# Performance work log

Measured on AMD Instinct MI355X. Metric: run time of the kernel, lower is better.

Reference implementation:

```python
import jax, jax.numpy as jnp
import numpy as np

NU, NI = 100000, 50000      # global embedding table sizes
U, I = 50000, 20000         # nodes in this subgraph
E = 400000                  # edges per direction
HID, H = 512, 8
D = HID // H                # out_feats per head = 64
NEG_SLOPE = 0.2


def setup_inputs() -> dict:
    key = jax.random.key(0)
    ks = jax.random.split(key, 16)
    s = 1.0 / np.sqrt(HID)
    a = 1.0 / np.sqrt(D)
    return {
        'u_gid': jax.random.randint(ks[0], (U,), 0, NU),
        'i_gid': jax.random.randint(ks[1], (I,), 0, NI),
        'src_u': jax.random.randint(ks[2], (E,), 0, U),
        'dst_i': jax.random.randint(ks[3], (E,), 0, I),
        'user_emb': jax.random.normal(ks[4], (NU, HID), jnp.float32) * 0.02,
        'item_emb': jax.random.normal(ks[5], (NI, HID), jnp.float32) * 0.02,
        # 'interact' (user -> item) GATConv params
        'W_ui': jax.random.normal(ks[6], (HID, HID), jnp.float32) * s,
        'al_ui': jax.random.normal(ks[7], (H, D), jnp.float32) * a,
        'ar_ui': jax.random.normal(ks[8], (H, D), jnp.float32) * a,
        'b_ui': jnp.zeros((HID,), jnp.float32),
        # 'interact_rev' (item -> user) GATConv params
        'W_iu': jax.random.normal(ks[9], (HID, HID), jnp.float32) * s,
        'al_iu': jax.random.normal(ks[10], (H, D), jnp.float32) * a,
        'ar_iu': jax.random.normal(ks[11], (H, D), jnp.float32) * a,
        'b_iu': jnp.zeros((HID,), jnp.float32),
    }


def gat_conv(h_src, h_dst, src, dst, W, attn_l, attn_r, bias, n_dst):
    """DGL GATConv (eval mode, allow_zero_in_degree): [n_dst, H, D]."""
    fs = (h_src @ W).reshape(-1, H, D)            # [Ns,H,D]
    fd = (h_dst @ W).reshape(-1, H, D)            # [Nd,H,D]
    el = jnp.sum(fs * attn_l, axis=-1)            # [Ns,H]
    er = jnp.sum(fd * attn_r, axis=-1)            # [Nd,H]
    e = jax.nn.leaky_relu(el[src] + er[dst], NEG_SLOPE)   # [E,H]
    # segment softmax over incoming edges of each destination
    emax = jax.ops.segment_max(e, dst, num_segments=n_dst)[dst]
    ex = jnp.exp(e - emax)                        # [E,H]
    denom = jax.ops.segment_sum(ex, dst, num_segments=n_dst)[dst]
    alpha = ex / denom                            # [E,H]
    msg = fs[src] * alpha[:, :, None]             # [E,H,D]
    out = jax.ops.segment_sum(msg, dst, num_segments=n_dst)  # zero for isolated dst
    return out + bias.reshape(1, H, D)


def reference(u_gid, i_gid, src_u, dst_i, user_emb, item_emb,
              W_ui, al_ui, ar_ui, b_ui, W_iu, al_iu, ar_iu, b_iu):
    h_u0 = user_emb[u_gid]                        # [U,HID]
    h_i0 = item_emb[i_gid]                        # [I,HID]
    # 'interact': user -> item
    h_item = gat_conv(h_u0, h_i0, src_u, dst_i, W_ui, al_ui, ar_ui, b_ui, I)
    # 'interact_rev': item -> user (reversed edges)
    h_user = gat_conv(h_i0, h_u0, dst_i, src_u, W_iu, al_iu, ar_iu, b_iu, U)
    h_user = h_user.reshape(U, HID)
    h_item = h_item.reshape(I, HID)
    item_mean = jnp.mean(h_item, axis=0, keepdims=True)        # [1,HID]
    item_expand = jnp.broadcast_to(item_mean, (U, HID))
    return jnp.concatenate([h_user, item_expand], axis=1)      # [U, 2*HID]
```

## Files before the change

### kernel.cpp

```cpp
#include <hip/hip_runtime.h>
#include <hip/hip_bf16.h>
#include <stdint.h>

#define U_NODES 50000
#define I_NODES 20000
#define N_NODES 70000
#define M_PAD   70016
#define E_EDGES 400000
#define HID     512

typedef __attribute__((ext_vector_type(8))) short short8;
typedef __attribute__((ext_vector_type(4))) float floatx4;

static __device__ __forceinline__ uint16_t f2b(float f) {
    uint32_t x = __float_as_uint(f);
    x += 0x7fffu + ((x >> 16) & 1u);
    return (uint16_t)(x >> 16);
}
static __device__ __forceinline__ float b2f(short u) {
    return __uint_as_float(((uint32_t)(uint16_t)u) << 16);
}

__global__ void gather_cast(const int* __restrict__ u_gid, const int* __restrict__ i_gid,
                            const float* __restrict__ user_emb, const float* __restrict__ item_emb,
                            uint16_t* __restrict__ Xb)
{
    int t = blockIdx.x * 256 + threadIdx.x;
    int n = t >> 7;
    int j = (t & 127) << 2;
    uint2 o;
    if (n < N_NODES) {
        const float* src = (n < U_NODES) ? (user_emb + (size_t)u_gid[n] * HID)
                                         : (item_emb + (size_t)i_gid[n - U_NODES] * HID);
        float4 v = *(const float4*)(src + j);
        o.x = (uint32_t)f2b(v.x) | ((uint32_t)f2b(v.y) << 16);
        o.y = (uint32_t)f2b(v.z) | ((uint32_t)f2b(v.w) << 16);
    } else { o.x = 0u; o.y = 0u; }
    *(uint2*)(Xb + (size_t)n * HID + j) = o;
}

__global__ void prep_w(const float* __restrict__ Wui, const float* __restrict__ Wiu,
                       uint16_t* __restrict__ Wt)
{
    int t = blockIdx.x * 256 + threadIdx.x;
    int n = t >> 9, k = t & 511;
    float v = (n < 512) ? Wui[k * 512 + n] : Wiu[k * 512 + (n - 512)];
    Wt[(size_t)n * 512 + k] = f2b(v);
}

__global__ __launch_bounds__(256) void gemm_bf16(const uint16_t* __restrict__ Xb,
                                                 const uint16_t* __restrict__ Wt,
                                                 const float* __restrict__ al_ui, const float* __restrict__ ar_ui,
                                                 const float* __restrict__ al_iu, const float* __restrict__ ar_iu,
                                                 uint16_t* __restrict__ F,
                                                 float* __restrict__ ELui, float* __restrict__ ERui,
                                                 float* __restrict__ ELiu, float* __restrict__ ERiu)
{
    __shared__ __align__(16) uint16_t As[2][128 * 32];
    __shared__ __align__(16) uint16_t Bs[2][128 * 32];
    const int tid = threadIdx.x;
    const int wave = tid >> 6, lane = tid & 63;

    int bid = blockIdx.x;
    int x = bid & 7, ii = bid >> 3;
    int L = x * 547 + ii;
    const int m0 = (L >> 3) * 128;
    const int n0 = (L & 7) * 128;
    const int wm = (wave & 1) * 64;
    const int wn = (wave >> 1) * 64;

    const int rl2 = lane >> 2;
    const int sg = ((lane & 3) ^ ((lane >> 3) & 3)) * 8;
    const int ca = wave * 2, cb = wave * 2 + 1;
    const uint16_t* gA0 = Xb + (size_t)(m0 + ca * 16 + rl2) * HID + sg;
    const uint16_t* gA1 = Xb + (size_t)(m0 + cb * 16 + rl2) * HID + sg;
    const uint16_t* gB0 = Wt + (size_t)(n0 + ca * 16 + rl2) * HID + sg;
    const uint16_t* gB1 = Wt + (size_t)(n0 + cb * 16 + rl2) * HID + sg;

    floatx4 zero = {0.f, 0.f, 0.f, 0.f};
    floatx4 acc[4][4];
    #pragma unroll
    for (int a = 0; a < 4; ++a)
        #pragma unroll
        for (int b = 0; b < 4; ++b) acc[a][b] = zero;

    const int r = lane & 15, quad = lane >> 4;
    const int slq8 = (quad ^ ((r >> 1) & 3)) * 8;

#define STAGE(KO, BUF) do {                                                                         \
    __builtin_amdgcn_global_load_lds((const __attribute__((address_space(1))) void*)(gA0 + (KO)),   \
                                     (__attribute__((address_space(3))) void*)(&As[BUF][ca * 512]), 16, 0, 0); \
    __builtin_amdgcn_global_load_lds((const __attribute__((address_space(1))) void*)(gA1 + (KO)),   \
                                     (__attribute__((address_space(3))) void*)(&As[BUF][cb * 512]), 16, 0, 0); \
    __builtin_amdgcn_global_load_lds((const __attribute__((address_space(1))) void*)(gB0 + (KO)),   \
                                     (__attribute__((address_space(3))) void*)(&Bs[BUF][ca * 512]), 16, 0, 0); \
    __builtin_amdgcn_global_load_lds((const __attribute__((address_space(1))) void*)(gB1 + (KO)),   \
                                     (__attribute__((address_space(3))) void*)(&Bs[BUF][cb * 512]), 16, 0, 0); \
} while (0)

#define COMPUTE(BUF) do {                                                                           \
    short8 af[4], bf[4];                                                                            \
    _Pragma("unroll")                                                                               \
    for (int tm = 0; tm < 4; ++tm)                                                                  \
        af[tm] = *(const short8*)&As[BUF][(wm + tm * 16 + r) * 32 + slq8];                          \
    _Pragma("unroll")                                                                               \
    for (int tn = 0; tn < 4; ++tn)                                                                  \
        bf[tn] = *(const short8*)&Bs[BUF][(wn + tn * 16 + r) * 32 + slq8];                          \
    _Pragma("unroll")                                                                               \
    for (int tm = 0; tm < 4; ++tm)                                                                  \
        _Pragma("unroll")                                                                           \
        for (int tn = 0; tn < 4; ++tn)                                                              \
            acc[tm][tn] = __builtin_amdgcn_mfma_f32_16x16x32_bf16(af[tm], bf[tn], acc[tm][tn], 0, 0, 0); \
} while (0)

    STAGE(0, 0);
    __syncthreads();
    #pragma unroll
    for (int t = 0; t < 15; ++t) {
        const int bc = t & 1;
        STAGE((t + 1) * 32, bc ^ 1);
        COMPUTE(bc);
        __syncthreads();
    }
    COMPUTE(1);

#undef STAGE
#undef COMPUTE

    const bool collo = (n0 < 512);
    const bool allU = (m0 + 128 <= U_NODES);
    const bool allI = (m0 >= U_NODES);
    const bool storeb = (allU && collo) || (allI && !collo) || (!allU && !allI);

    const int colh = n0 + wn;
    const int h = (colh & 511) >> 6;
    const float* arv = collo ? ar_ui : ar_iu;
    float* ERp = collo ? ERui : ERiu;
    float ar4[4];
    #pragma unroll
    for (int tn = 0; tn < 4; ++tn) ar4[tn] = arv[h * 64 + tn * 16 + r];

    if (storeb) {
        const float* alv = collo ? al_ui : al_iu;
        float* ELp = collo ? ELui : ELiu;
        float al4[4];
        #pragma unroll
        for (int tn = 0; tn < 4; ++tn) al4[tn] = alv[h * 64 + tn * 16 + r];
        #pragma unroll
        for (int tm = 0; tm < 4; ++tm) {
            #pragma unroll
            for (int rr = 0; rr < 4; ++rr) {
                int row = m0 + wm + tm * 16 + quad * 4 + rr;
                float sl = 0.f, sr = 0.f;
                #pragma unroll
                for (int tn = 0; tn < 4; ++tn) {
                    sl += acc[tm][tn][rr] * al4[tn];
                    sr += acc[tm][tn][rr] * ar4[tn];
                }
                if (row < N_NODES && ((row < U_NODES) == collo)) {
                    #pragma unroll
                    for (int tn = 0; tn < 4; ++tn) {
                        int col = n0 + wn + tn * 16 + r;
                        F[(size_t)row * 1024 + col] = f2b(acc[tm][tn][rr]);
                    }
                }
                #pragma unroll
                for (int d = 1; d < 16; d <<= 1) {
                    sl += __shfl_xor(sl, d);
                    sr += __shfl_xor(sr, d);
                }
                if (r == 0 && row < N_NODES) {
                    ELp[row * 8 + h] = sl;
                    ERp[row * 8 + h] = sr;
                }
            }
        }
    } else {
        #pragma unroll
        for (int tm = 0; tm < 4; ++tm) {
            #pragma unroll
            for (int rr = 0; rr < 4; ++rr) {
                int row = m0 + wm + tm * 16 + quad * 4 + rr;
                float sr = 0.f;
                #pragma unroll
                for (int tn = 0; tn < 4; ++tn) sr += acc[tm][tn][rr] * ar4[tn];
                #pragma unroll
                for (int d = 1; d < 16; d <<= 1) sr += __shfl_xor(sr, d);
                if (r == 0 && row < N_NODES) ERp[row * 8 + h] = sr;
            }
        }
    }
}

__global__ void hist_kernel(const int* __restrict__ src_u, const int* __restrict__ dst_i,
                            int* __restrict__ counts_i, int* __restrict__ counts_u)
{
    int e = blockIdx.x * 256 + threadIdx.x;
    if (e >= E_EDGES) return;
    atomicAdd(&counts_i[dst_i[e]], 1);
    atomicAdd(&counts_u[src_u[e]], 1);
}

__global__ __launch_bounds__(1024) void scan_kernel(const int* __restrict__ counts_i,
                                                    const int* __restrict__ counts_u,
                                                    int* __restrict__ offs_i, int* __restrict__ cur_i,
                                                    int* __restrict__ offs_u, int* __restrict__ cur_u)
{
    const int* counts; int n; int* offs; int* cur;
    if (blockIdx.x == 0) { counts = counts_i; n = I_NODES; offs = offs_i; cur = cur_i; }
    else                 { counts = counts_u; n = U_NODES; offs = offs_u; cur = cur_u; }
    __shared__ int wsum[16];
    int tid = threadIdx.x, lane = tid & 63, w = tid >> 6;
    int carry = 0;
    for (int base = 0; base < n; base += 1024) {
        int i = base + tid;
        int v = (i < n) ? counts[i] : 0;
        int x = v;
        #pragma unroll
        for (int d = 1; d < 64; d <<= 1) {
            int y = __shfl_up(x, d, 64);
            if (lane >= d) x += y;
        }
        if (lane == 63) wsum[w] = x;
        __syncthreads();
        if (w == 0) {
            int s = (lane < 16) ? wsum[lane] : 0;
            #pragma unroll
            for (int d = 1; d < 16; d <<= 1) {
                int y = __shfl_up(s, d, 16);
                if ((lane & 15) >= d) s += y;
            }
            if (lane < 16) wsum[lane] = s;
        }
        __syncthreads();
        int wexcl = (w == 0) ? 0 : wsum[w - 1];
        int excl = carry + wexcl + (x - v);
        if (i < n) { offs[i] = excl; cur[i] = excl; }
        int tot = wsum[15];
        __syncthreads();
        carry += tot;
    }
    if (tid == 0) offs[n] = carry;
}

__global__ void scatter_kernel(const int* __restrict__ src_u, const int* __restrict__ dst_i,
                               int* __restrict__ cur_i, int* __restrict__ cur_u,
                               int* __restrict__ sorted_ui, int* __restrict__ sorted_iu,
                               const float* __restrict__ ELui, const float* __restrict__ ERui,
                               const float* __restrict__ ELiu, const float* __restrict__ ERiu,
                               float* __restrict__ ex_ui, float* __restrict__ ex_iu)
{
    int e = blockIdx.x * 256 + threadIdx.x;
    if (e >= E_EDGES) return;
    int s = src_u[e], d = dst_i[e];
    int dn = U_NODES + d;
    int p = atomicAdd(&cur_i[d], 1);
    int q = atomicAdd(&cur_u[s], 1);
    sorted_ui[p] = s;
    sorted_iu[q] = dn;
    #pragma unroll
    for (int h = 0; h < 8; ++h) {
        float e1 = ELui[s * 8 + h] + ERui[dn * 8 + h];
        e1 = (e1 >= 0.f) ? e1 : 0.2f * e1;
        ex_ui[(size_t)p * 8 + h] = __expf(e1);
        float e2 = ELiu[dn * 8 + h] + ERiu[s * 8 + h];
        e2 = (e2 >= 0.f) ? e2 : 0.2f * e2;
        ex_iu[(size_t)q * 8 + h] = __expf(e2);
    }
}

#define IBLK ((I_NODES + 3) / 4)
#define UBLK ((U_NODES + 3) / 4)
__global__ __launch_bounds__(256) void agg3_kernel(
    const int* __restrict__ offs_i, const int* __restrict__ sorted_ui, const float* __restrict__ ex_ui,
    const int* __restrict__ offs_u, const int* __restrict__ sorted_iu, const float* __restrict__ ex_iu,
    const uint16_t* __restrict__ F, const float* __restrict__ b_iu,
    float* __restrict__ out, float* __restrict__ itemF)
{
    int bid = blockIdx.x;
    int w = threadIdx.x >> 6, lane = threadIdx.x & 63;
    bool item_mode = bid < IBLK;
    const int* offs; const int* srcs; const float* ex; int dst, colbase, n_dst;
    if (item_mode) { offs = offs_i; srcs = sorted_ui; ex = ex_ui; dst = bid * 4 + w;          colbase = 0;   n_dst = I_NODES; }
    else           { offs = offs_u; srcs = sorted_iu; ex = ex_iu; dst = (bid - IBLK) * 4 + w; colbase = 512; n_dst = U_NODES; }
    if (dst >= n_dst) return;
    int h = lane >> 3;
    int j0 = offs[dst], j1 = offs[dst + 1];

    float den = 0.f;
    float acc[8] = {0.f, 0.f, 0.f, 0.f, 0.f, 0.f, 0.f, 0.f};
    const int fb = colbase + lane * 8;
    int j = j0;
    for (; j + 8 <= j1; j += 8) {
        int s[8]; float wt[8]; short8 f[8];
        #pragma unroll
        for (int i = 0; i < 8; ++i) s[i] = srcs[j + i];
        #pragma unroll
        for (int i = 0; i < 8; ++i) wt[i] = ex[(size_t)(j + i) * 8 + h];
        #pragma unroll
        for (int i = 0; i < 8; ++i) f[i] = *(const short8*)&F[(size_t)s[i] * 1024 + fb];
        #pragma unroll
        for (int i = 0; i < 8; ++i) {
            den += wt[i];
            #pragma unroll
            for (int q = 0; q < 8; ++q) acc[q] += wt[i] * b2f(f[i][q]);
        }
    }
    for (; j + 4 <= j1; j += 4) {
        int s[4]; float wt[4]; short8 f[4];
        #pragma unroll
        for (int i = 0; i < 4; ++i) s[i] = srcs[j + i];
        #pragma unroll
        for (int i = 0; i < 4; ++i) wt[i] = ex[(size_t)(j + i) * 8 + h];
        #pragma unroll
        for (int i = 0; i < 4; ++i) f[i] = *(const short8*)&F[(size_t)s[i] * 1024 + fb];
        #pragma unroll
        for (int i = 0; i < 4; ++i) {
            den += wt[i];
            #pragma unroll
            for (int q = 0; q < 8; ++q) acc[q] += wt[i] * b2f(f[i][q]);
        }
    }
    for (; j < j1; ++j) {
        int s0 = srcs[j];
        float w0 = ex[(size_t)j * 8 + h];
        short8 f0 = *(const short8*)&F[(size_t)s0 * 1024 + fb];
        den += w0;
        #pragma unroll
        for (int q = 0; q < 8; ++q) acc[q] += w0 * b2f(f0[q]);
    }
    float inv = (j1 > j0) ? (1.f / den) : 0.f;
    #pragma unroll
    for (int q = 0; q < 8; ++q) acc[q] *= inv;

    int col = lane * 8;
    if (item_mode) {
        float* o = itemF + (size_t)dst * 512 + col;
        float4 v0 = {acc[0], acc[1], acc[2], acc[3]};
        float4 v1 = {acc[4], acc[5], acc[6], acc[7]};
        *(float4*)(o + 0) = v0;
        *(float4*)(o + 4) = v1;
    } else {
        float* o = out + (size_t)dst * 1024 + col;
        float4 v0 = {acc[0] + b_iu[col + 0], acc[1] + b_iu[col + 1],
                     acc[2] + b_iu[col + 2], acc[3] + b_iu[col + 3]};
        float4 v1 = {acc[4] + b_iu[col + 4], acc[5] + b_iu[col + 5],
                     acc[6] + b_iu[col + 6], acc[7] + b_iu[col + 7]};
        *(float4*)(o + 0) = v0;
        *(float4*)(o + 4) = v1;
    }
}

__global__ void item_reduce(const float* __restrict__ itemF, float* __restrict__ partial2)
{
    int b = blockIdx.x;
    int t = threadIdx.x;
    int cg = (t & 127) * 4;
    int rp = t >> 7;
    float4 s = {0.f, 0.f, 0.f, 0.f};
    int r0 = b * 500;
    for (int r = r0 + rp; r < r0 + 500; r += 2) {
        float4 v = *(const float4*)&itemF[(size_t)r * 512 + cg];
        s.x += v.x; s.y += v.y; s.z += v.z; s.w += v.w;
    }
    *(float4*)&partial2[(size_t)(b * 2 + rp) * 512 + cg] = s;
}

__global__ void meanvec_kernel(const float* __restrict__ partial2, const float* __restrict__ b_ui,
                               float* __restrict__ mean_vec)
{
    int c = threadIdx.x;
    float s = 0.f;
    for (int p = 0; p < 80; ++p) s += partial2[p * 512 + c];
    mean_vec[c] = s * (1.0f / (float)I_NODES) + b_ui[c];
}

__global__ void bcast_kernel(const float* __restrict__ mean_vec, float* __restrict__ out)
{
    int t = blockIdx.x * 256 + threadIdx.x;
    int u = t >> 7, q = t & 127;
    float4 v = ((const float4*)mean_vec)[q];
    *(float4*)(out + (size_t)u * 1024 + 512 + q * 4) = v;
}

extern "C" void kernel_launch(void* const* d_in, const int* in_sizes, int n_in,
                              void* d_out, int out_size, void* d_ws, size_t ws_size,
                              hipStream_t stream)
{
    const int*   u_gid    = (const int*)d_in[0];
    const int*   i_gid    = (const int*)d_in[1];
    const int*   src_u    = (const int*)d_in[2];
    const int*   dst_i    = (const int*)d_in[3];
    const float* user_emb = (const float*)d_in[4];
    const float* item_emb = (const float*)d_in[5];
    const float* W_ui     = (const float*)d_in[6];
    const float* al_ui    = (const float*)d_in[7];
    const float* ar_ui    = (const float*)d_in[8];
    const float* b_ui     = (const float*)d_in[9];
    const float* W_iu     = (const float*)d_in[10];
    const float* al_iu    = (const float*)d_in[11];
    const float* ar_iu    = (const float*)d_in[12];
    const float* b_iu     = (const float*)d_in[13];
    float* out = (float*)d_out;

    char* ws = (char*)d_ws;
    size_t off = 0;
    auto alloc = [&](size_t bytes) -> void* {
        void* p = ws + off;
        off = (off + bytes + 255) & ~(size_t)255;
        return p;
    };
    uint16_t* Xb   = (uint16_t*)alloc((size_t)M_PAD * 512 * 2);
    uint16_t* Wt   = (uint16_t*)alloc((size_t)1024 * 512 * 2);
    uint16_t* F    = (uint16_t*)alloc((size_t)M_PAD * 1024 * 2);
    float* ELui    = (float*)alloc((size_t)N_NODES * 8 * 4);
    float* ERui    = (float*)alloc((size_t)N_NODES * 8 * 4);
    float* ELiu    = (float*)alloc((size_t)N_NODES * 8 * 4);
    float* ERiu    = (float*)alloc((size_t)N_NODES * 8 * 4);
    int* offs_i    = (int*)alloc((size_t)(I_NODES + 1) * 4);
    int* cur_i     = (int*)alloc((size_t)I_NODES * 4);
    int* offs_u    = (int*)alloc((size_t)(U_NODES + 1) * 4);
    int* cur_u     = (int*)alloc((size_t)U_NODES * 4);
    int* sorted_ui = (int*)alloc((size_t)E_EDGES * 4);
    int* sorted_iu = (int*)alloc((size_t)E_EDGES * 4);
    float* ex_ui   = (float*)alloc((size_t)E_EDGES * 8 * 4);
    float* ex_iu   = (float*)alloc((size_t)E_EDGES * 8 * 4);
    float* itemF   = (float*)alloc((size_t)I_NODES * 512 * 4);
    float* partial2= (float*)alloc((size_t)80 * 512 * 4);
    char* zptr = ws + off;
    int*   counts_i = (int*)alloc((size_t)I_NODES * 4);
    int*   counts_u = (int*)alloc((size_t)U_NODES * 4);
    size_t zbytes = (size_t)((ws + off) - zptr);
    float* mean_vec = (float*)alloc(512 * 4);
    (void)ws_size; (void)in_sizes; (void)n_in; (void)out_size;

    hipMemsetAsync(zptr, 0, zbytes, stream);
    prep_w<<<2048, 256, 0, stream>>>(W_ui, W_iu, Wt);
    gather_cast<<<M_PAD * 128 / 256, 256, 0, stream>>>(u_gid, i_gid, user_emb, item_emb, Xb);
    gemm_bf16<<<(M_PAD / 128) * 8, 256, 0, stream>>>(Xb, Wt, al_ui, ar_ui, al_iu, ar_iu,
                                                     F, ELui, ERui, ELiu, ERiu);
    hist_kernel<<<(E_EDGES + 255) / 256, 256, 0, stream>>>(src_u, dst_i, counts_i, counts_u);
    scan_kernel<<<2, 1024, 0, stream>>>(counts_i, counts_u, offs_i, cur_i, offs_u, cur_u);
    scatter_kernel<<<(E_EDGES + 255) / 256, 256, 0, stream>>>(src_u, dst_i, cur_i, cur_u,
                                                              sorted_ui, sorted_iu,
                                                              ELui, ERui, ELiu, ERiu,
                                                              ex_ui, ex_iu);
    agg3_kernel<<<IBLK + UBLK, 256, 0, stream>>>(offs_i, sorted_ui, ex_ui,
                                                 offs_u, sorted_iu, ex_iu,
                                                 F, b_iu, out, itemF);
    item_reduce<<<40, 256, 0, stream>>>(itemF, partial2);
    meanvec_kernel<<<1, 512, 0, stream>>>(partial2, b_ui, mean_vec);
    bcast_kernel<<<U_NODES * 128 / 256, 256, 0, stream>>>(mean_vec, out);
}
```

Measured before the change: 880.1 us.

## Recompute edge attention in aggregation, parallelize scan, widen item reduction

Drops the per-edge exp buffers written by the scatter kernel; the aggregation kernel now recomputes leaky-relu/exp weights from per-node EL/ER tables using the destination's ER value. The two-block serial prefix scan is replaced with a three-pass multi-block scan, and the item mean reduction uses four times as many blocks. This removes a large per-edge write/read and a serialized scan, at the cost of extra gathers of source EL values and redundant exp per lane in aggregation.

Measured after the change: 775.9 us. 1.13x faster.

```diff
diff --git a/kernel.cpp b/kernel.cpp
--- a/kernel.cpp
+++ b/kernel.cpp
@@ -201,91 +201,128 @@
     atomicAdd(&counts_u[src_u[e]], 1);
 }
 
-__global__ __launch_bounds__(1024) void scan_kernel(const int* __restrict__ counts_i,
-                                                    const int* __restrict__ counts_u,
-                                                    int* __restrict__ offs_i, int* __restrict__ cur_i,
-                                                    int* __restrict__ offs_u, int* __restrict__ cur_u)
-{
-    const int* counts; int n; int* offs; int* cur;
-    if (blockIdx.x == 0) { counts = counts_i; n = I_NODES; offs = offs_i; cur = cur_i; }
-    else                 { counts = counts_u; n = U_NODES; offs = offs_u; cur = cur_u; }
-    __shared__ int wsum[16];
-    int tid = threadIdx.x, lane = tid & 63, w = tid >> 6;
-    int carry = 0;
-    for (int base = 0; base < n; base += 1024) {
-        int i = base + tid;
-        int v = (i < n) ? counts[i] : 0;
-        int x = v;
-        #pragma unroll
-        for (int d = 1; d < 64; d <<= 1) {
-            int y = __shfl_up(x, d, 64);
-            if (lane >= d) x += y;
-        }
-        if (lane == 63) wsum[w] = x;
-        __syncthreads();
-        if (w == 0) {
-            int s = (lane < 16) ? wsum[lane] : 0;
-            #pragma unroll
-            for (int d = 1; d < 16; d <<= 1) {
-                int y = __shfl_up(s, d, 16);
-                if ((lane & 15) >= d) s += y;
-            }
-            if (lane < 16) wsum[lane] = s;
-        }
-        __syncthreads();
-        int wexcl = (w == 0) ? 0 : wsum[w - 1];
-        int excl = carry + wexcl + (x - v);
+#define SCAN_CHUNK 1024
+#define IBLKS ((I_NODES + SCAN_CHUNK - 1) / SCAN_CHUNK)
+#define UBLKS ((U_NODES + SCAN_CHUNK - 1) / SCAN_CHUNK)
+
+__global__ __launch_bounds__(256) void scan_level1(const int* __restrict__ counts_i,
+                                                   const int* __restrict__ counts_u,
+                                                   int* __restrict__ bsum)
+{
+    int b = blockIdx.x, t = threadIdx.x;
+    const int* cnt; int n, base;
+    if (b < IBLKS) { cnt = counts_i; n = I_NODES; base = b * SCAN_CHUNK; }
+    else           { cnt = counts_u; n = U_NODES; base = (b - IBLKS) * SCAN_CHUNK; }
+    int idx = base + t * 4;
+    int s = 0;
+    #pragma unroll
+    for (int k = 0; k < 4; ++k) { int i = idx + k; if (i < n) s += cnt[i]; }
+    __shared__ int ws[4];
+    int lane = t & 63, w = t >> 6;
+    int xv = s;
+    #pragma unroll
+    for (int d = 1; d < 64; d <<= 1) xv += __shfl_xor(xv, d);
+    if (lane == 0) ws[w] = xv;
+    __syncthreads();
+    if (t == 0) bsum[b] = ws[0] + ws[1] + ws[2] + ws[3];
+}
+
+__global__ void scan_level2(const int* __restrict__ bsum, int* __restrict__ boff,
+                            int* __restrict__ offs_i, int* __restrict__ offs_u)
+{
+    int t = threadIdx.x;
+    int w = t >> 6, lane = t & 63;
+    if (w == 0) {
+        int v = (lane < IBLKS) ? bsum[lane] : 0;
+        int xv = v;
+        #pragma unroll
+        for (int d = 1; d < 64; d <<= 1) { int y = __shfl_up(xv, d, 64); if (lane >= d) xv += y; }
+        if (lane < IBLKS) boff[lane] = xv - v;
+        if (lane == IBLKS - 1) offs_i[I_NODES] = xv;
+    } else {
+        int v = (lane < UBLKS) ? bsum[IBLKS + lane] : 0;
+        int xv = v;
+        #pragma unroll
+        for (int d = 1; d < 64; d <<= 1) { int y = __shfl_up(xv, d, 64); if (lane >= d) xv += y; }
+        if (lane < UBLKS) boff[IBLKS + lane] = xv - v;
+        if (lane == UBLKS - 1) offs_u[U_NODES] = xv;
+    }
+}
+
+__global__ __launch_bounds__(256) void scan_level3(const int* __restrict__ counts_i,
+                                                   const int* __restrict__ counts_u,
+                                                   const int* __restrict__ boff,
+                                                   int* __restrict__ offs_i, int* __restrict__ cur_i,
+                                                   int* __restrict__ offs_u, int* __restrict__ cur_u)
+{
+    int b = blockIdx.x, t = threadIdx.x;
+    const int* cnt; int n, base; int* offs; int* cur;
+    if (b < IBLKS) { cnt = counts_i; n = I_NODES; base = b * SCAN_CHUNK; offs = offs_i; cur = cur_i; }
+    else           { cnt = counts_u; n = U_NODES; base = (b - IBLKS) * SCAN_CHUNK; offs = offs_u; cur = cur_u; }
+    int idx = base + t * 4;
+    int v[4]; int s = 0;
+    #pragma unroll
+    for (int k = 0; k < 4; ++k) { int i = idx + k; v[k] = (i < n) ? cnt[i] : 0; s += v[k]; }
+    __shared__ int ws[4];
+    int lane = t & 63, w = t >> 6;
+    int xv = s;
+    #pragma unroll
+    for (int d = 1; d < 64; d <<= 1) { int y = __shfl_up(xv, d, 64); if (lane >= d) xv += y; }
+    if (lane == 63) ws[w] = xv;
+    __syncthreads();
+    int wexcl = 0;
+    #pragma unroll
+    for (int k = 0; k < 4; ++k) if (k < w) wexcl += ws[k];
+    int excl = boff[b] + wexcl + (xv - s);
+    #pragma unroll
+    for (int k = 0; k < 4; ++k) {
+        int i = idx + k;
         if (i < n) { offs[i] = excl; cur[i] = excl; }
-        int tot = wsum[15];
-        __syncthreads();
-        carry += tot;
-    }
-    if (tid == 0) offs[n] = carry;
+        excl += v[k];
+    }
 }
 
 __global__ void scatter_kernel(const int* __restrict__ src_u, const int* __restrict__ dst_i,
                                int* __restrict__ cur_i, int* __restrict__ cur_u,
-                               int* __restrict__ sorted_ui, int* __restrict__ sorted_iu,
-                               const float* __restrict__ ELui, const float* __restrict__ ERui,
-                               const float* __restrict__ ELiu, const float* __restrict__ ERiu,
-                               float* __restrict__ ex_ui, float* __restrict__ ex_iu)
+                               int* __restrict__ sorted_ui, int* __restrict__ sorted_iu)
 {
     int e = blockIdx.x * 256 + threadIdx.x;
     if (e >= E_EDGES) return;
     int s = src_u[e], d = dst_i[e];
-    int dn = U_NODES + d;
     int p = atomicAdd(&cur_i[d], 1);
     int q = atomicAdd(&cur_u[s], 1);
     sorted_ui[p] = s;
-    sorted_iu[q] = dn;
-    #pragma unroll
-    for (int h = 0; h < 8; ++h) {
-        float e1 = ELui[s * 8 + h] + ERui[dn * 8 + h];
-        e1 = (e1 >= 0.f) ? e1 : 0.2f * e1;
-        ex_ui[(size_t)p * 8 + h] = __expf(e1);
-        float e2 = ELiu[dn * 8 + h] + ERiu[s * 8 + h];
-        e2 = (e2 >= 0.f) ? e2 : 0.2f * e2;
-        ex_iu[(size_t)q * 8 + h] = __expf(e2);
-    }
+    sorted_iu[q] = U_NODES + d;
 }
 
 #define IBLK ((I_NODES + 3) / 4)
 #define UBLK ((U_NODES + 3) / 4)
 __global__ __launch_bounds__(256) void agg3_kernel(
-    const int* __restrict__ offs_i, const int* __restrict__ sorted_ui, const float* __restrict__ ex_ui,
-    const int* __restrict__ offs_u, const int* __restrict__ sorted_iu, const float* __restrict__ ex_iu,
+    const int* __restrict__ offs_i, const int* __restrict__ sorted_ui,
+    const int* __restrict__ offs_u, const int* __restrict__ sorted_iu,
+    const float* __restrict__ ELui, const float* __restrict__ ERui,
+    const float* __restrict__ ELiu, const float* __restrict__ ERiu,
     const uint16_t* __restrict__ F, const float* __restrict__ b_iu,
     float* __restrict__ out, float* __restrict__ itemF)
 {
     int bid = blockIdx.x;
     int w = threadIdx.x >> 6, lane = threadIdx.x & 63;
     bool item_mode = bid < IBLK;
-    const int* offs; const int* srcs; const float* ex; int dst, colbase, n_dst;
-    if (item_mode) { offs = offs_i; srcs = sorted_ui; ex = ex_ui; dst = bid * 4 + w;          colbase = 0;   n_dst = I_NODES; }
-    else           { offs = offs_u; srcs = sorted_iu; ex = ex_iu; dst = (bid - IBLK) * 4 + w; colbase = 512; n_dst = U_NODES; }
+    const int* offs; const int* srcs; const float* el_tab; const float* er_tab;
+    int dst, colbase, n_dst, dstnode;
+    if (item_mode) {
+        offs = offs_i; srcs = sorted_ui; el_tab = ELui; er_tab = ERui;
+        dst = bid * 4 + w; colbase = 0; n_dst = I_NODES;
+        dstnode = U_NODES + dst;
+    } else {
+        offs = offs_u; srcs = sorted_iu; el_tab = ELiu; er_tab = ERiu;
+        dst = (bid - IBLK) * 4 + w; colbase = 512; n_dst = U_NODES;
+        dstnode = dst;
+    }
     if (dst >= n_dst) return;
     int h = lane >> 3;
     int j0 = offs[dst], j1 = offs[dst + 1];
+    float er_h = er_tab[dstnode * 8 + h];
 
     float den = 0.f;
     float acc[8] = {0.f, 0.f, 0.f, 0.f, 0.f, 0.f, 0.f, 0.f};
@@ -296,7 +333,11 @@
         #pragma unroll
         for (int i = 0; i < 8; ++i) s[i] = srcs[j + i];
         #pragma unroll
-        for (int i = 0; i < 8; ++i) wt[i] = ex[(size_t)(j + i) * 8 + h];
+        for (int i = 0; i < 8; ++i) {
+            float e0 = el_tab[s[i] * 8 + h] + er_h;
+            e0 = (e0 >= 0.f) ? e0 : 0.2f * e0;
+            wt[i] = __expf(e0);
+        }
         #pragma unroll
         for (int i = 0; i < 8; ++i) f[i] = *(const short8*)&F[(size_t)s[i] * 1024 + fb];
         #pragma unroll
@@ -311,7 +352,11 @@
         #pragma unroll
         for (int i = 0; i < 4; ++i) s[i] = srcs[j + i];
         #pragma unroll
-        for (int i = 0; i < 4; ++i) wt[i] = ex[(size_t)(j + i) * 8 + h];
+        for (int i = 0; i < 4; ++i) {
+            float e0 = el_tab[s[i] * 8 + h] + er_h;
+            e0 = (e0 >= 0.f) ? e0 : 0.2f * e0;
+            wt[i] = __expf(e0);
+        }
         #pragma unroll
         for (int i = 0; i < 4; ++i) f[i] = *(const short8*)&F[(size_t)s[i] * 1024 + fb];
         #pragma unroll
@@ -323,7 +368,9 @@
     }
     for (; j < j1; ++j) {
         int s0 = srcs[j];
-        float w0 = ex[(size_t)j * 8 + h];
+        float e0 = el_tab[s0 * 8 + h] + er_h;
+        e0 = (e0 >= 0.f) ? e0 : 0.2f * e0;
+        float w0 = __expf(e0);
         short8 f0 = *(const short8*)&F[(size_t)s0 * 1024 + fb];
         den += w0;
         #pragma unroll
@@ -358,8 +405,8 @@
     int cg = (t & 127) * 4;
     int rp = t >> 7;
     float4 s = {0.f, 0.f, 0.f, 0.f};
-    int r0 = b * 500;
-    for (int r = r0 + rp; r < r0 + 500; r += 2) {
+    int r0 = b * 125;
+    for (int r = r0 + rp; r < r0 + 125; r += 2) {
         float4 v = *(const float4*)&itemF[(size_t)r * 512 + cg];
         s.x += v.x; s.y += v.y; s.z += v.z; s.w += v.w;
     }
@@ -371,7 +418,7 @@
 {
     int c = threadIdx.x;
     float s = 0.f;
-    for (int p = 0; p < 80; ++p) s += partial2[p * 512 + c];
+    for (int p = 0; p < 320; ++p) s += partial2[p * 512 + c];
     mean_vec[c] = s * (1.0f / (float)I_NODES) + b_ui[c];
 }
 
@@ -423,10 +470,10 @@
     int* cur_u     = (int*)alloc((size_t)U_NODES * 4);
     int* sorted_ui = (int*)alloc((size_t)E_EDGES * 4);
     int* sorted_iu = (int*)alloc((size_t)E_EDGES * 4);
-    float* ex_ui   = (float*)alloc((size_t)E_EDGES * 8 * 4);
-    float* ex_iu   = (float*)alloc((size_t)E_EDGES * 8 * 4);
+    int* bsum      = (int*)alloc((size_t)(IBLKS + UBLKS) * 4);
+    int* boff      = (int*)alloc((size_t)(IBLKS + UBLKS) * 4);
     float* itemF   = (float*)alloc((size_t)I_NODES * 512 * 4);
-    float* partial2= (float*)alloc((size_t)80 * 512 * 4);
+    float* partial2= (float*)alloc((size_t)320 * 512 * 4);
     char* zptr = ws + off;
     int*   counts_i = (int*)alloc((size_t)I_NODES * 4);
     int*   counts_u = (int*)alloc((size_t)U_NODES * 4);
@@ -440,15 +487,16 @@
     gemm_bf16<<<(M_PAD / 128) * 8, 256, 0, stream>>>(Xb, Wt, al_ui, ar_ui, al_iu, ar_iu,
                                                      F, ELui, ERui, ELiu, ERiu);
     hist_kernel<<<(E_EDGES + 255) / 256, 256, 0, stream>>>(src_u, dst_i, counts_i, counts_u);
-    scan_kernel<<<2, 1024, 0, stream>>>(counts_i, counts_u, offs_i, cur_i, offs_u, cur_u);
+    scan_level1<<<IBLKS + UBLKS, 256, 0, stream>>>(counts_i, counts_u, bsum);
+    scan_level2<<<1, 128, 0, stream>>>(bsum, boff, offs_i, offs_u);
+    scan_level3<<<IBLKS + UBLKS, 256, 0, stream>>>(counts_i, counts_u, boff,
+                                                   offs_i, cur_i, offs_u, cur_u);
     scatter_kernel<<<(E_EDGES + 255) / 256, 256, 0, stream>>>(src_u, dst_i, cur_i, cur_u,
-                                                              sorted_ui, sorted_iu,
-                                                              ELui, ERui, ELiu, ERiu,
-                                                              ex_ui, ex_iu);
-    agg3_kernel<<<IBLK + UBLK, 256, 0, stream>>>(offs_i, sorted_ui, ex_ui,
-                                                 offs_u, sorted_iu, ex_iu,
+                                                              sorted_ui, sorted_iu);
+    agg3_kernel<<<IBLK + UBLK, 256, 0, stream>>>(offs_i, sorted_ui, offs_u, sorted_iu,
+                                                 ELui, ERui, ELiu, ERiu,
                                                  F, b_iu, out, itemF);
-    item_reduce<<<40, 256, 0, stream>>>(itemF, partial2);
+    item_reduce<<<160, 256, 0, stream>>>(itemF, partial2);
     meanvec_kernel<<<1, 512, 0, stream>>>(partial2, b_ui, mean_vec);
     bcast_kernel<<<U_NODES * 128 / 256, 256, 0, stream>>>(mean_vec, out);
 }
```
